# Performance work log

Hardware: AMD Instinct MI355X
Metric: run time of the kernel (lower is better)

## Reference

```python
import jax, jax.numpy as jnp
import numpy as np

ALPHA = 9.0
EPS = 2.220446049250313e-16  # sys.float_info.epsilon
N, K = 131072, 256


def setup_inputs() -> dict:
    key = jax.random.key(0)
    k1, k2 = jax.random.split(key)
    latent_view_1 = jax.random.uniform(k1, (N, K), dtype=jnp.float32)
    latent_view_2 = jax.random.uniform(k2, (N, K), dtype=jnp.float32)
    return {"latent_view_1": latent_view_1, "latent_view_2": latent_view_2}


def reference(latent_view_1, latent_view_2):
    # joint: sum_n v1[n,i] * v2[n,j]  == v1^T @ v2  (rank-N GEMM, [k,k] output)
    p_i_j = jnp.einsum('ni,nj->ij', latent_view_1, latent_view_2)
    p_i_j = (p_i_j + p_i_j.T) / 2.0
    p_i_j = p_i_j / jnp.sum(p_i_j)
    p_i = jnp.sum(p_i_j, axis=1, keepdims=True)  # [k,1] marginal
    p_j = jnp.sum(p_i_j, axis=0, keepdims=True)  # [1,k] marginal
    p_i_j = jnp.maximum(p_i_j, EPS)
    p_i = jnp.maximum(p_i, EPS)
    p_j = jnp.maximum(p_j, EPS)
    loss = -p_i_j * (jnp.log(p_i_j)
                     - (ALPHA + 1.0) * jnp.log(p_j)
                     - (ALPHA + 1.0) * jnp.log(p_i))
    return jnp.sum(loss)
```

## Files before the change

### kernel.cpp

```cpp
#include <hip/hip_runtime.h>
#include <hip/hip_bf16.h>

#define KDIM 256
#define NTOT 131072
#define PN   65536
#define NB   256
#define RPB  512
#define NCH  16
#define CH   (32*KDIM)

typedef float f32x4 __attribute__((ext_vector_type(4)));
typedef __bf16 bf16x8 __attribute__((ext_vector_type(8)));

__device__ __forceinline__ unsigned short f2bf(float x){
  unsigned u = __float_as_uint(x);
  u += 0x7fffu + ((u >> 16) & 1u);
  return (unsigned short)(u >> 16);
}
__device__ __forceinline__ unsigned pk2(float lo, float hi){
  return (unsigned)f2bf(lo) | ((unsigned)f2bf(hi) << 16);
}
__device__ __forceinline__ float bf2f(unsigned short u){
  return __uint_as_float((unsigned)u << 16);
}
__device__ __forceinline__ int swz(int i){ return (((i >> 1) ^ (i >> 4)) & 7) << 4; }

struct Stage { f32x4 a0, a1, b0, b1; };

__device__ __forceinline__ void stage_load(Stage& s, const float* pa, const float* pb, long off){
  s.a0 = *(const f32x4*)(pa + off);
  s.a1 = *(const f32x4*)(pa + off + KDIM);
  s.b0 = *(const f32x4*)(pb + off);
  s.b1 = *(const f32x4*)(pb + off + KDIM);
}

__device__ __forceinline__ void stage_store(const Stage& s, char* As, char* Bs, const int* offW){
#pragma unroll
  for (int m = 0; m < 4; ++m){
    *(unsigned*)(As + offW[m]) = pk2(s.a0[m], s.a1[m]);
    *(unsigned*)(Bs + offW[m]) = pk2(s.b0[m], s.b1[m]);
  }
}

__device__ __forceinline__ void compute_t(const char* As, const char* Bs,
                                          const int* offA, const int* offB,
                                          f32x4 (&acc)[4][4])
{
  bf16x8 af[4], bfr[4];
#pragma unroll
  for (int m = 0; m < 4; ++m) af[m]  = *(const bf16x8*)(As + offA[m]);
#pragma unroll
  for (int n = 0; n < 4; ++n) bfr[n] = *(const bf16x8*)(Bs + offB[n]);
#pragma unroll
  for (int m = 0; m < 4; ++m)
#pragma unroll
    for (int n = 0; n < 4; ++n)
      acc[m][n] = __builtin_amdgcn_mfma_f32_16x16x32_bf16(af[m], bfr[n], acc[m][n], 0, 0, 0);
}

__global__ __launch_bounds__(1024) void k_gemm(const float* __restrict__ v1,
                                               const float* __restrict__ v2,
                                               unsigned short* __restrict__ part)
{
  __shared__ char sm[65536];
  const int t    = threadIdx.x;
  const int b    = blockIdx.x;
  const int lane = t & 63, wid = t >> 6;
  const int di   = lane & 15, g = lane >> 4;
  const int wr   = wid >> 2, wc = wid & 3;
  const int i0   = wr * 64, j0 = wc * 64;
  const int rp   = wid;
  const int c0   = lane * 4;

  int offW[4], offA[4], offB[4];
#pragma unroll
  for (int m = 0; m < 4; ++m){ int i = c0 + m;         offW[m] = ((i << 6) + (rp << 2)) ^ swz(i); }
#pragma unroll
  for (int m = 0; m < 4; ++m){ int i = i0 + 16*m + di; offA[m] = ((i << 6) + (g << 4)) ^ swz(i); }
#pragma unroll
  for (int n = 0; n < 4; ++n){ int j = j0 + 16*n + di; offB[n] = ((j << 6) + (g << 4)) ^ swz(j); }

  f32x4 acc[4][4];
#pragma unroll
  for (int m = 0; m < 4; ++m)
#pragma unroll
    for (int n = 0; n < 4; ++n){ f32x4 z = {0.f,0.f,0.f,0.f}; acc[m][n] = z; }

  const long rowBase = (long)b * RPB;
  const float* pa = v1 + (rowBase + 2*rp) * KDIM + c0;
  const float* pb = v2 + (rowBase + 2*rp) * KDIM + c0;

  Stage s;
  stage_load(s, pa, pb, 0);
  stage_store(s, sm, sm + 16384, offW);
  asm volatile("s_waitcnt lgkmcnt(0)");
  __builtin_amdgcn_sched_barrier(0);
  __builtin_amdgcn_s_barrier();

#pragma unroll 1
  for (int c = 0; c < NCH; ++c){
    const int cb = c & 1;
    char* Ac = sm + cb * 32768;        char* Bc = Ac + 16384;
    char* An = sm + (cb ^ 1) * 32768;  char* Bn = An + 16384;
    if (c + 1 < NCH){
      stage_load(s, pa, pb, (long)(c + 1) * CH);
      __builtin_amdgcn_sched_barrier(0);
    }
    compute_t(Ac, Bc, offA, offB, acc);
    __builtin_amdgcn_sched_barrier(0);
    if (c + 1 < NCH){
      stage_store(s, An, Bn, offW);
    }
    asm volatile("s_waitcnt lgkmcnt(0)");
    __builtin_amdgcn_sched_barrier(0);
    __builtin_amdgcn_s_barrier();
  }

  unsigned short* op = part + (size_t)b * PN;
#pragma unroll
  for (int m = 0; m < 4; ++m)
#pragma unroll
    for (int n = 0; n < 4; ++n){
      const int i = i0 + 16*m + 4*g;
      const int j = j0 + 16*n + di;
#pragma unroll
      for (int r = 0; r < 4; ++r)
        op[(size_t)(i + r) * KDIM + j] = f2bf(acc[m][n][r]);
    }
}

__global__ __launch_bounds__(1024) void k_reduce(const unsigned short* __restrict__ part,
                                                 float* __restrict__ P,
                                                 float* __restrict__ rsum,
                                                 float* __restrict__ csum)
{
  __shared__ float red[1024];
  const int gr = blockIdx.x;
  const int t  = threadIdx.x;
  const int j  = t & 255, q = t >> 8;
  const int bpq = NB >> 2;
  float s = 0.f;
  const unsigned short* p = part + (size_t)(q * bpq) * PN + gr * KDIM + j;
  for (int b = 0; b < bpq; ++b) s += bf2f(p[(size_t)b * PN]);
  red[t] = s; __syncthreads();
  if (t < 512) red[t] += red[t + 512];
  __syncthreads();
  float v = 0.f;
  if (t < 256){
    v = red[t] + red[t + 256];
    P[gr * KDIM + t] = v;
    atomicAdd(&csum[t], v);
  }
  __syncthreads();
  red[t] = (t < 256) ? v : 0.f;
  __syncthreads();
  for (int st = 128; st > 0; st >>= 1){
    if (t < st) red[t] += red[t + st];
    __syncthreads();
  }
  if (t == 0) rsum[gr] = red[0];
}

__global__ __launch_bounds__(256) void k_marg(const float* __restrict__ rsum,
                                              const float* __restrict__ csum,
                                              float* __restrict__ lm,
                                              float* __restrict__ scal,
                                              float* __restrict__ out)
{
  __shared__ float red[256];
  const int i = threadIdx.x;
  float ri = rsum[i];
  red[i] = ri; __syncthreads();
  for (int st = 128; st > 0; st >>= 1){
    if (i < st) red[i] += red[i + st];
    __syncthreads();
  }
  const float S = red[0];
  const float inv2S = 0.5f / S;
  float mi = (ri + csum[i]) * inv2S;
  mi = fmaxf(mi, 2.220446049250313e-16f);
  lm[i] = logf(mi);
  if (i == 0){ scal[0] = inv2S; out[0] = 0.f; }
}

__global__ __launch_bounds__(256) void k_loss(const float* __restrict__ P,
                                              const float* __restrict__ lm,
                                              const float* __restrict__ scal,
                                              float* __restrict__ out)
{
  __shared__ float red[256];
  const float inv2S = scal[0];
  float acc = 0.f;
  const int base = blockIdx.x * 512;
  for (int e = base + threadIdx.x; e < base + 512; e += 256){
    const int i = e >> 8, j = e & 255;
    float q = (P[i * KDIM + j] + P[j * KDIM + i]) * inv2S;
    q = fmaxf(q, 2.220446049250313e-16f);
    acc += -q * (logf(q) - 10.0f * (lm[i] + lm[j]));
  }
  red[threadIdx.x] = acc; __syncthreads();
  for (int st = 128; st > 0; st >>= 1){
    if (threadIdx.x < st) red[threadIdx.x] += red[threadIdx.x + st];
    __syncthreads();
  }
  if (threadIdx.x == 0) atomicAdd(out, red[0]);
}

extern "C" void kernel_launch(void* const* d_in, const int* in_sizes, int n_in,
                              void* d_out, int out_size, void* d_ws, size_t ws_size,
                              hipStream_t stream) {
  const float* v1 = (const float*)d_in[0];
  const float* v2 = (const float*)d_in[1];
  float* out = (float*)d_out;
  char*  wsc = (char*)d_ws;

  unsigned short* part = (unsigned short*)wsc;
  float* P    = (float*)(wsc + (size_t)NB * PN * 2);
  float* rsum = P + PN;
  float* csum = rsum + 256;
  float* lm   = csum + 256;
  float* scal = lm + 256;

  hipMemsetAsync(csum, 0, 256 * sizeof(float), stream);
  k_gemm  <<<NB, 1024, 0, stream>>>(v1, v2, part);
  k_reduce<<<256, 1024, 0, stream>>>(part, P, rsum, csum);
  k_marg  <<<1, 256, 0, stream>>>(rsum, csum, lm, scal, out);
  k_loss  <<<128, 256, 0, stream>>>(P, lm, scal, out);
}
```

Measured before the change: 75.06 us.

## Deepen GEMM global-load prefetch and split loader threads per input matrix

The GEMM's global-to-LDS staging is rebuilt. Each half of the block now loads one input matrix, in 16-row chunks, with two chunks of registers kept in flight instead of one. The loop writes the next tile's two halves to LDS and issues loads two chunks ahead before running the MFMA on the current tile, with a peeled tail for the last two tiles. The aim is to hide HBM latency in what is largely a bandwidth-bound streaming GEMM. The cost is more live registers and a more complex schedule.

New measurement: 79.17 us. 1.05x slower.

```diff
diff --git a/kernel.cpp b/kernel.cpp
--- a/kernel.cpp
+++ b/kernel.cpp
@@ -6,8 +6,9 @@
 #define PN   65536
 #define NB   256
 #define RPB  512
-#define NCH  16
-#define CH   (32*KDIM)
+#define CHROWS 16
+#define CH   (CHROWS*KDIM)
+#define NTL  16
 
 typedef float f32x4 __attribute__((ext_vector_type(4)));
 typedef __bf16 bf16x8 __attribute__((ext_vector_type(8)));
@@ -25,21 +26,17 @@
 }
 __device__ __forceinline__ int swz(int i){ return (((i >> 1) ^ (i >> 4)) & 7) << 4; }
 
-struct Stage { f32x4 a0, a1, b0, b1; };
-
-__device__ __forceinline__ void stage_load(Stage& s, const float* pa, const float* pb, long off){
-  s.a0 = *(const f32x4*)(pa + off);
-  s.a1 = *(const f32x4*)(pa + off + KDIM);
-  s.b0 = *(const f32x4*)(pb + off);
-  s.b1 = *(const f32x4*)(pb + off + KDIM);
-}
-
-__device__ __forceinline__ void stage_store(const Stage& s, char* As, char* Bs, const int* offW){
-#pragma unroll
-  for (int m = 0; m < 4; ++m){
-    *(unsigned*)(As + offW[m]) = pk2(s.a0[m], s.a1[m]);
-    *(unsigned*)(Bs + offW[m]) = pk2(s.b0[m], s.b1[m]);
-  }
+struct Stage { f32x4 r0, r1; };
+
+__device__ __forceinline__ void stage_load(Stage& s, const float* src, long off){
+  s.r0 = *(const f32x4*)(src + off);
+  s.r1 = *(const f32x4*)(src + off + KDIM);
+}
+
+__device__ __forceinline__ void stage_store(const Stage& s, char* tile, const int* offW){
+#pragma unroll
+  for (int m = 0; m < 4; ++m)
+    *(unsigned*)(tile + offW[m]) = pk2(s.r0[m], s.r1[m]);
 }
 
 __device__ __forceinline__ void compute_t(const char* As, const char* Bs,
@@ -56,6 +53,14 @@
 #pragma unroll
     for (int n = 0; n < 4; ++n)
       acc[m][n] = __builtin_amdgcn_mfma_f32_16x16x32_bf16(af[m], bfr[n], acc[m][n], 0, 0, 0);
+}
+
+__device__ __forceinline__ void lds_fence_barrier(){
+  __builtin_amdgcn_sched_barrier(0);
+  asm volatile("s_waitcnt lgkmcnt(0)");
+  __builtin_amdgcn_sched_barrier(0);
+  __builtin_amdgcn_s_barrier();
+  __builtin_amdgcn_sched_barrier(0);
 }
 
 __global__ __launch_bounds__(1024) void k_gemm(const float* __restrict__ v1,
@@ -69,12 +74,21 @@
   const int di   = lane & 15, g = lane >> 4;
   const int wr   = wid >> 2, wc = wid & 3;
   const int i0   = wr * 64, j0 = wc * 64;
-  const int rp   = wid;
-  const int c0   = lane * 4;
-
-  int offW[4], offA[4], offB[4];
-#pragma unroll
-  for (int m = 0; m < 4; ++m){ int i = c0 + m;         offW[m] = ((i << 6) + (rp << 2)) ^ swz(i); }
+
+  const int mtx = t >> 9;
+  const int p   = (t >> 6) & 7;
+  const int q   = t & 63;
+  const float* src = (mtx ? v2 : v1) + ((long)b * RPB + 2 * p) * KDIM + 4 * q;
+  const int sbase = mtx * 16384;
+
+  int offW0[4], offW1[4], offA[4], offB[4];
+#pragma unroll
+  for (int m = 0; m < 4; ++m){
+    const int i   = 4*q + m;
+    const int lin = (i << 6) + (p << 2);
+    offW0[m] = sbase + ( lin        ^ swz(i));
+    offW1[m] = sbase + ((lin + 32)  ^ swz(i));
+  }
 #pragma unroll
   for (int m = 0; m < 4; ++m){ int i = i0 + 16*m + di; offA[m] = ((i << 6) + (g << 4)) ^ swz(i); }
 #pragma unroll
@@ -86,34 +100,43 @@
 #pragma unroll
     for (int n = 0; n < 4; ++n){ f32x4 z = {0.f,0.f,0.f,0.f}; acc[m][n] = z; }
 
-  const long rowBase = (long)b * RPB;
-  const float* pa = v1 + (rowBase + 2*rp) * KDIM + c0;
-  const float* pb = v2 + (rowBase + 2*rp) * KDIM + c0;
-
-  Stage s;
-  stage_load(s, pa, pb, 0);
-  stage_store(s, sm, sm + 16384, offW);
-  asm volatile("s_waitcnt lgkmcnt(0)");
-  __builtin_amdgcn_sched_barrier(0);
-  __builtin_amdgcn_s_barrier();
-
-#pragma unroll 1
-  for (int c = 0; c < NCH; ++c){
-    const int cb = c & 1;
-    char* Ac = sm + cb * 32768;        char* Bc = Ac + 16384;
-    char* An = sm + (cb ^ 1) * 32768;  char* Bn = An + 16384;
-    if (c + 1 < NCH){
-      stage_load(s, pa, pb, (long)(c + 1) * CH);
-      __builtin_amdgcn_sched_barrier(0);
-    }
-    compute_t(Ac, Bc, offA, offB, acc);
-    __builtin_amdgcn_sched_barrier(0);
-    if (c + 1 < NCH){
-      stage_store(s, An, Bn, offW);
-    }
-    asm volatile("s_waitcnt lgkmcnt(0)");
-    __builtin_amdgcn_sched_barrier(0);
-    __builtin_amdgcn_s_barrier();
+  Stage S0, S1;
+  stage_load(S0, src, 0L * CH);
+  stage_load(S1, src, 1L * CH);
+  stage_store(S0, sm, offW0);
+  __builtin_amdgcn_sched_barrier(0);
+  stage_load(S0, src, 2L * CH);
+  __builtin_amdgcn_sched_barrier(0);
+  stage_store(S1, sm, offW1);
+  __builtin_amdgcn_sched_barrier(0);
+  stage_load(S1, src, 3L * CH);
+  lds_fence_barrier();
+
+#pragma unroll 2
+  for (int it = 0; it < NTL - 2; ++it){
+    char* Tc = sm + (it & 1) * 32768;
+    char* Tn = sm + ((it + 1) & 1) * 32768;
+    stage_store(S0, Tn, offW0);
+    __builtin_amdgcn_sched_barrier(0);
+    stage_load(S0, src, (long)(2*it + 4) * CH);
+    __builtin_amdgcn_sched_barrier(0);
+    stage_store(S1, Tn, offW1);
+    __builtin_amdgcn_sched_barrier(0);
+    stage_load(S1, src, (long)(2*it + 5) * CH);
+    __builtin_amdgcn_sched_barrier(0);
+    compute_t(Tc, Tc + 16384, offA, offB, acc);
+    lds_fence_barrier();
+  }
+
+  {
+    char* Tc = sm + ((NTL - 2) & 1) * 32768;
+    char* Tn = sm + ((NTL - 1) & 1) * 32768;
+    stage_store(S0, Tn, offW0);
+    stage_store(S1, Tn, offW1);
+    __builtin_amdgcn_sched_barrier(0);
+    compute_t(Tc, Tc + 16384, offA, offB, acc);
+    lds_fence_barrier();
+    compute_t(Tn, Tn + 16384, offA, offB, acc);
   }
 
   unsigned short* op = part + (size_t)b * PN;
```
